# Performance work log

Hardware: AMD Instinct MI355X
Metric: run time of the kernel (lower is better)

The kernel has to match this reference:

```python
import jax, jax.numpy as jnp
import numpy as np

EPS = 1e-6

def setup_inputs() -> dict:
    key = jax.random.key(0)
    ks = jax.random.split(key, 9)
    B, H, M = 8192, 1024, 16
    Hh = H // 2
    s = lambda k, shape, fan: jax.random.normal(k, shape, jnp.float32) * (1.0 / np.sqrt(fan))
    return {
        "query_embedding": jax.random.normal(ks[0], (B, H), jnp.float32),
        "cls1_w": s(ks[1], (Hh, H), H),
        "cls1_b": jnp.zeros((Hh,), jnp.float32),
        "cls3_w": s(ks[2], (M, Hh), Hh),
        "cls3_b": jnp.zeros((M,), jnp.float32),
        "exp_w1": s(ks[3], (M, Hh, H), H),
        "exp_b1": jnp.zeros((M, Hh), jnp.float32),
        "exp_w2": s(ks[4], (M, H, Hh), Hh),
        "exp_b2": jnp.zeros((M, H), jnp.float32),
    }

def _l2_normalize(x, eps=EPS):
    # F.normalize: x / clamp(||x||_2, min=eps)
    n = jnp.sqrt(jnp.sum(x * x, axis=-1, keepdims=True))
    return x / jnp.maximum(n, eps)

def reference(query_embedding, cls1_w, cls1_b, cls3_w, cls3_b,
              exp_w1, exp_b1, exp_w2, exp_b2):
    q = query_embedding  # [B, H]
    # --- cls(): gating network (eval, sbmoe_top1) ---
    x1 = jax.nn.relu(q @ cls1_w.T + cls1_b)          # [B, H/2]
    logits = x1 @ cls3_w.T + cls3_b                  # [B, M]
    probs = jax.nn.softmax(logits, axis=-1)          # [B, M]
    top1 = jnp.argmax(probs, axis=-1)                # [B]
    mask = jax.nn.one_hot(top1, probs.shape[-1], dtype=probs.dtype)
    gates = probs * mask                             # [B, M] (one nonzero/row)
    # --- query_embedder(): run all experts, gate, combine ---
    h = jax.nn.relu(jnp.einsum('bd,mhd->bmh', q, exp_w1) + exp_b1)   # [B, M, H/2]
    expert_out = jnp.einsum('bmh,mdh->bmd', h, exp_w2) + exp_b2      # [B, M, H]
    combined = jnp.einsum('bmd,bm->bd', expert_out, gates)           # [B, H]
    out = _l2_normalize(combined) + q
    return out
```

## Files before the change

### kernel.cpp

```cpp
#include <hip/hip_runtime.h>
#include <math.h>

#define NB 8192
#define H 1024
#define HH 512
#define NEXP 16
#define NT128 96
#define AMBIG_THR 1e-3f

typedef __attribute__((ext_vector_type(8))) short bfrag;
typedef __attribute__((ext_vector_type(4))) float f4;

__device__ __forceinline__ f4 MF(bfrag a, bfrag b, f4 c) {
    return __builtin_amdgcn_mfma_f32_16x16x32_bf16(a, b, c, 0, 0, 0);
}
__device__ __forceinline__ unsigned short f2bf(float f) {
    unsigned u = __float_as_uint(f);
    u += 0x7fff + ((u >> 16) & 1);
    return (unsigned short)(u >> 16);
}
__device__ __forceinline__ float bf2f(unsigned short h) {
    return __uint_as_float((unsigned)h << 16);
}

typedef __attribute__((address_space(1))) const unsigned GAS;
typedef __attribute__((address_space(3))) unsigned LAS;
__device__ __forceinline__ void gld16(const void* g, void* l) {
    __builtin_amdgcn_global_load_lds((GAS*)g, (LAS*)l, 16, 0, 0);
}

__global__ __launch_bounds__(256) void cvtA_kernel(
    const float* __restrict__ q, const float* __restrict__ w1, const float* __restrict__ w3,
    unsigned short* __restrict__ qhi, unsigned short* __restrict__ qlo,
    unsigned short* __restrict__ w1hi, unsigned short* __restrict__ w1lo,
    unsigned short* __restrict__ w3hi, unsigned short* __restrict__ w3lo,
    int* __restrict__ counts, int* __restrict__ ambig_cnt)
{
    const int b = blockIdx.x, t = threadIdx.x;
    if (b == 0) {
        if (t < NEXP) counts[t] = 0;
        if (t == NEXP) ambig_cnt[0] = 0;
    }
    const float* src; unsigned short *hi, *lo; int i;
    if (b < 8192)      { src = q;  hi = qhi;  lo = qlo;  i = b * 256 + t; }
    else if (b < 8704) { src = w1; hi = w1hi; lo = w1lo; i = (b - 8192) * 256 + t; }
    else               { src = w3; hi = w3hi; lo = w3lo; i = (b - 8704) * 256 + t; }
    float4 v = ((const float4*)src)[i];
    ushort4 h, l;
    h.x = f2bf(v.x); l.x = f2bf(v.x - bf2f(h.x));
    h.y = f2bf(v.y); l.y = f2bf(v.y - bf2f(h.y));
    h.z = f2bf(v.z); l.z = f2bf(v.z - bf2f(h.z));
    h.w = f2bf(v.w); l.w = f2bf(v.w - bf2f(h.w));
    ((ushort4*)hi)[i] = h;
    ((ushort4*)lo)[i] = l;
}

__global__ __launch_bounds__(256) void cvtB_kernel(
    const float* __restrict__ ew1, const float* __restrict__ ew2,
    unsigned short* __restrict__ d1, unsigned short* __restrict__ d2)
{
    const int b = blockIdx.x, t = threadIdx.x;
    const float* src; unsigned short* dst; int i;
    if (b < 8192) { src = ew1; dst = d1; i = b * 256 + t; }
    else          { src = ew2; dst = d2; i = (b - 8192) * 256 + t; }
    float4 v = ((const float4*)src)[i];
    ushort4 h;
    h.x = f2bf(v.x); h.y = f2bf(v.y); h.z = f2bf(v.z); h.w = f2bf(v.w);
    ((ushort4*)dst)[i] = h;
}

__global__ __launch_bounds__(512) void g1_kernel(
    const unsigned short* __restrict__ qhi, const unsigned short* __restrict__ qlo,
    const unsigned short* __restrict__ w1hi, const unsigned short* __restrict__ w1lo,
    const float* __restrict__ b1,
    unsigned short* __restrict__ x1hi, unsigned short* __restrict__ x1lo)
{
    __shared__ unsigned short Ah[3][128][32];
    __shared__ unsigned short Al[3][128][32];
    __shared__ unsigned short Bh[3][128][32];
    __shared__ unsigned short Bl[3][128][32];

    const int t = threadIdx.x, w = t >> 6, lane = t & 63;
    const int quad = lane >> 4, l16 = lane & 15;
    const int wr = w & 3, wc = w >> 2;
    const int rowA0 = blockIdx.x * 128;
    const int colB0 = blockIdx.y * 128;
    const int rl = lane >> 2, sl = lane & 3;

    const unsigned short* gsrc[4];
    unsigned short* lbase[4];
    #pragma unroll
    for (int j = 0; j < 4; ++j) {
        int c = w + j * 8;
        int rloc; const unsigned short* s; unsigned short* d;
        if (c < 8)       { rloc = c * 16 + rl;        s = qhi  + (size_t)(rowA0 + rloc) * H; d = &Ah[0][c * 16][0]; }
        else if (c < 16) { rloc = (c - 8) * 16 + rl;  s = qlo  + (size_t)(rowA0 + rloc) * H; d = &Al[0][(c - 8) * 16][0]; }
        else if (c < 24) { rloc = (c - 16) * 16 + rl; s = w1hi + (size_t)(colB0 + rloc) * H; d = &Bh[0][(c - 16) * 16][0]; }
        else             { rloc = (c - 24) * 16 + rl; s = w1lo + (size_t)(colB0 + rloc) * H; d = &Bl[0][(c - 24) * 16][0]; }
        int f = (rloc & 3) ^ ((rloc >> 2) & 3);
        gsrc[j]  = s + (sl ^ f) * 8;
        lbase[j] = d;
    }
    const int bstr = 128 * 32;

    const f4 z4 = {0.f, 0.f, 0.f, 0.f};
    f4 acc[2][4] = {{z4, z4, z4, z4}, {z4, z4, z4, z4}};
    const int sw = (quad ^ (l16 & 3) ^ (l16 >> 2)) * 8;
    const int ra0 = wr * 32 + l16, ra1 = ra0 + 16;
    const int cbase = wc * 64;

    auto STAGE = [&](int buf, int kt) {
        #pragma unroll
        for (int j = 0; j < 4; ++j)
            gld16(gsrc[j] + kt * 32, lbase[j] + buf * bstr);
    };
    auto COMPUTE = [&](int buf) {
        bfrag ah0 = *(const bfrag*)&Ah[buf][ra0][sw];
        bfrag al0 = *(const bfrag*)&Al[buf][ra0][sw];
        bfrag ah1 = *(const bfrag*)&Ah[buf][ra1][sw];
        bfrag al1 = *(const bfrag*)&Al[buf][ra1][sw];
        #pragma unroll
        for (int cb = 0; cb < 4; ++cb) {
            bfrag bh = *(const bfrag*)&Bh[buf][cbase + cb * 16 + l16][sw];
            bfrag bl = *(const bfrag*)&Bl[buf][cbase + cb * 16 + l16][sw];
            acc[0][cb] = MF(al0, bh, MF(ah0, bl, MF(ah0, bh, acc[0][cb])));
            acc[1][cb] = MF(al1, bh, MF(ah1, bl, MF(ah1, bh, acc[1][cb])));
        }
    };

    STAGE(0, 0);
    STAGE(1, 1);
    for (int kt = 0; kt < 32; ++kt) {
        if (kt < 31) asm volatile("s_waitcnt vmcnt(4)" ::: "memory");
        else         asm volatile("s_waitcnt vmcnt(0)" ::: "memory");
        __builtin_amdgcn_s_barrier();
        if (kt < 30) STAGE((kt + 2) % 3, kt + 2);
        COMPUTE(kt % 3);
    }

    const int row0 = rowA0 + wr * 32;
    #pragma unroll
    for (int cb = 0; cb < 4; ++cb) {
        int col = colB0 + cbase + cb * 16 + l16;
        float bias = b1[col];
        #pragma unroll
        for (int rb = 0; rb < 2; ++rb)
            #pragma unroll
            for (int i = 0; i < 4; ++i) {
                int row = rb * 16 + quad * 4 + i;
                float v = fmaxf(acc[rb][cb][i] + bias, 0.f);
                unsigned short hh = f2bf(v);
                size_t idx = (size_t)(row0 + row) * HH + col;
                x1hi[idx] = hh;
                x1lo[idx] = f2bf(v - bf2f(hh));
            }
    }
}

__global__ __launch_bounds__(256) void logits_kernel(
    const unsigned short* __restrict__ x1hi, const unsigned short* __restrict__ x1lo,
    const unsigned short* __restrict__ w3hi, const unsigned short* __restrict__ w3lo,
    const float* __restrict__ b3,
    int* __restrict__ top1, float* __restrict__ gval, int* __restrict__ counts,
    int* __restrict__ ambig_rows, int* __restrict__ ambig_cnt)
{
    __shared__ float lgp[4][32][NEXP];
    const int t = threadIdx.x, wave = t >> 6, lane = t & 63;
    const int quad = lane >> 4, l16 = lane & 15;
    const int row0 = blockIdx.x * 32;
    const f4 z4 = {0.f, 0.f, 0.f, 0.f};

    f4 l0 = z4, l1 = z4;
    const size_t ar0 = (size_t)(row0 + l16) * HH + quad * 8;
    const size_t ar1 = ar0 + (size_t)16 * HH;
    const size_t br = (size_t)l16 * HH + quad * 8;
    #pragma unroll
    for (int ks = 0; ks < 4; ++ks) {
        int kk = wave * 128 + ks * 32;
        bfrag ah0 = *(const bfrag*)(x1hi + ar0 + kk);
        bfrag al0 = *(const bfrag*)(x1lo + ar0 + kk);
        bfrag ah1 = *(const bfrag*)(x1hi + ar1 + kk);
        bfrag al1 = *(const bfrag*)(x1lo + ar1 + kk);
        bfrag bh  = *(const bfrag*)(w3hi + br + kk);
        bfrag bl  = *(const bfrag*)(w3lo + br + kk);
        l0 = MF(al0, bh, MF(ah0, bl, MF(ah0, bh, l0)));
        l1 = MF(al1, bh, MF(ah1, bl, MF(ah1, bh, l1)));
    }
    #pragma unroll
    for (int i = 0; i < 4; ++i) {
        lgp[wave][quad * 4 + i][l16] = l0[i];
        lgp[wave][16 + quad * 4 + i][l16] = l1[i];
    }
    __syncthreads();

    if (t < 32) {
        float lg[NEXP];
        #pragma unroll
        for (int m = 0; m < NEXP; ++m)
            lg[m] = lgp[0][t][m] + lgp[1][t][m] + lgp[2][t][m] + lgp[3][t][m] + b3[m];
        float best = lg[0], second = -3.4e38f; int bi = 0;
        #pragma unroll
        for (int m = 1; m < NEXP; ++m) {
            float v = lg[m];
            if (v > best) { second = best; best = v; bi = m; }
            else if (v > second) second = v;
        }
        float se = 0.f;
        #pragma unroll
        for (int m = 0; m < NEXP; ++m) se += expf(lg[m] - best);
        int grow = row0 + t;
        top1[grow] = bi;
        gval[grow] = 1.f / se;
        atomicAdd(&counts[bi], 1);
        if (best - second < AMBIG_THR) {
            int pos = atomicAdd(ambig_cnt, 1);
            if (pos < NB) ambig_rows[pos] = grow;
        }
    }
}

__global__ __launch_bounds__(256) void fixup1_kernel(
    const float* __restrict__ q, const float* __restrict__ w1, const float* __restrict__ b1,
    const int* __restrict__ ambig_rows, const int* __restrict__ ambig_cnt,
    float* __restrict__ x1buf)
{
    __shared__ __align__(16) float qrow[H];
    const int t = threadIdx.x, wv = t >> 6, ln = t & 63;
    const int chunk = blockIdx.x & 7;
    const int slot  = blockIdx.x >> 3;
    const int base  = chunk * 64;
    int nn = *ambig_cnt; if (nn > NB) nn = NB;
    for (int ii = slot; ii < nn; ii += 32) {
        int row = ambig_rows[ii];
        ((float4*)qrow)[t] = ((const float4*)(q + (size_t)row * H))[t];
        __syncthreads();
        for (int c = base + wv * 2; c < base + 64; c += 8) {
            const float4* w0 = (const float4*)(w1 + (size_t)c * H);
            const float4* w1r = (const float4*)(w1 + (size_t)(c + 1) * H);
            const float4* qv = (const float4*)qrow;
            float s0 = 0.f, s1 = 0.f;
            #pragma unroll
            for (int j = 0; j < 4; ++j) {
                float4 a = qv[j * 64 + ln];
                float4 b0 = w0[j * 64 + ln];
                float4 b1v = w1r[j * 64 + ln];
                s0 += a.x * b0.x + a.y * b0.y + a.z * b0.z + a.w * b0.w;
                s1 += a.x * b1v.x + a.y * b1v.y + a.z * b1v.z + a.w * b1v.w;
            }
            #pragma unroll
            for (int off = 32; off; off >>= 1) {
                s0 += __shfl_xor(s0, off, 64);
                s1 += __shfl_xor(s1, off, 64);
            }
            if (ln == 0) {
                x1buf[(size_t)ii * HH + c]     = fmaxf(s0 + b1[c], 0.f);
                x1buf[(size_t)ii * HH + c + 1] = fmaxf(s1 + b1[c + 1], 0.f);
            }
        }
        __syncthreads();
    }
}

__global__ __launch_bounds__(256) void fixup2_kernel(
    const float* __restrict__ x1buf,
    const float* __restrict__ w3, const float* __restrict__ b3,
    const int* __restrict__ ambig_rows, const int* __restrict__ ambig_cnt,
    int* __restrict__ top1, float* __restrict__ gval, int* __restrict__ counts)
{
    __shared__ float lgs[NEXP];
    const int t = threadIdx.x, wv = t >> 6, ln = t & 63;
    int nn = *ambig_cnt; if (nn > NB) nn = NB;
    for (int ii = blockIdx.x; ii < nn; ii += gridDim.x) {
        int row = ambig_rows[ii];
        const float4* xv = (const float4*)(x1buf + (size_t)ii * HH);
        for (int m = wv; m < NEXP; m += 4) {
            const float4* wr = (const float4*)(w3 + (size_t)m * HH);
            float s = 0.f;
            #pragma unroll
            for (int j = 0; j < 2; ++j) {
                float4 a = xv[j * 64 + ln];
                float4 b = wr[j * 64 + ln];
                s += a.x * b.x + a.y * b.y + a.z * b.z + a.w * b.w;
            }
            #pragma unroll
            for (int off = 32; off; off >>= 1) s += __shfl_xor(s, off, 64);
            if (ln == 0) lgs[m] = s + b3[m];
        }
        __syncthreads();
        if (t == 0) {
            float best = lgs[0]; int bi = 0;
            #pragma unroll
            for (int m = 1; m < NEXP; ++m) if (lgs[m] > best) { best = lgs[m]; bi = m; }
            float se = 0.f;
            #pragma unroll
            for (int m = 0; m < NEXP; ++m) se += expf(lgs[m] - best);
            int old = top1[row];
            if (bi != old) {
                atomicSub(&counts[old], 1);
                atomicAdd(&counts[bi], 1);
                top1[row] = bi;
            }
            gval[row] = 1.f / se;
        }
        __syncthreads();
    }
}

__global__ __launch_bounds__(256) void osc_kernel(
    const int* __restrict__ counts,
    int* __restrict__ tm_e, int* __restrict__ tm_p, int* __restrict__ tm_end,
    const int* __restrict__ top1, int* __restrict__ brows)
{
    __shared__ int sbpos[NEXP];
    const int t = threadIdx.x;
    if (t == 0) {
        int run = 0, tile = 0;
        for (int e = 0; e < NEXP; ++e) {
            sbpos[e] = run;
            int beg = run, end = run + counts[e];
            for (int p = beg; p < end; p += 128) {
                tm_e[tile] = e; tm_p[tile] = p; tm_end[tile] = end; ++tile;
            }
            run = end;
        }
        for (; tile < NT128; ++tile) tm_e[tile] = -1;
    }
    __syncthreads();
    for (int i = t; i < NB; i += 256) {
        int e = top1[i];
        int pos = atomicAdd(&sbpos[e], 1);
        brows[pos] = i;
    }
}

__global__ __launch_bounds__(512) void exp1_kernel(
    const unsigned short* __restrict__ qb, const unsigned short* __restrict__ ew1b,
    const float* __restrict__ eb1,
    const int* __restrict__ tm_e, const int* __restrict__ tm_p, const int* __restrict__ tm_end,
    const int* __restrict__ brows, unsigned short* __restrict__ h)
{
    const int e = tm_e[blockIdx.x];
    if (e < 0) return;
    const int p0 = tm_p[blockIdx.x], end = tm_end[blockIdx.x];

    __shared__ unsigned short A[3][128][32];
    __shared__ unsigned short B[3][128][32];

    const int t = threadIdx.x, w = t >> 6, lane = t & 63;
    const int quad = lane >> 4, l16 = lane & 15;
    const int wr = w & 3, wc = w >> 2;
    const int c0 = blockIdx.y * 128;
    const unsigned short* w1p = ew1b + (size_t)e * HH * H;
    const int rl = lane >> 2, sl = lane & 3;

    const unsigned short* gsrc[2];
    unsigned short* lbase[2];
    #pragma unroll
    for (int j = 0; j < 2; ++j) {
        int c = w + j * 8;
        int rloc; const unsigned short* s; unsigned short* d;
        if (c < 8) {
            rloc = c * 16 + rl;
            int pa = p0 + rloc; if (pa >= end) pa = end - 1;
            s = qb + (size_t)brows[pa] * H;
            d = &A[0][c * 16][0];
        } else {
            rloc = (c - 8) * 16 + rl;
            s = w1p + (size_t)(c0 + rloc) * H;
            d = &B[0][(c - 8) * 16][0];
        }
        int f = (rloc & 3) ^ ((rloc >> 2) & 3);
        gsrc[j]  = s + (sl ^ f) * 8;
        lbase[j] = d;
    }
    const int bstr = 128 * 32;

    const f4 z4 = {0.f, 0.f, 0.f, 0.f};
    f4 acc[2][4] = {{z4, z4, z4, z4}, {z4, z4, z4, z4}};
    const int sw = (quad ^ (l16 & 3) ^ (l16 >> 2)) * 8;
    const int ra0 = wr * 32 + l16, ra1 = ra0 + 16;
    const int cbase = wc * 64;

    auto STAGE = [&](int buf, int kt) {
        #pragma unroll
        for (int j = 0; j < 2; ++j)
            gld16(gsrc[j] + kt * 32, lbase[j] + buf * bstr);
    };
    auto COMPUTE = [&](int buf) {
        bfrag a0 = *(const bfrag*)&A[buf][ra0][sw];
        bfrag a1 = *(const bfrag*)&A[buf][ra1][sw];
        #pragma unroll
        for (int cb = 0; cb < 4; ++cb) {
            bfrag bb = *(const bfrag*)&B[buf][cbase + cb * 16 + l16][sw];
            acc[0][cb] = MF(a0, bb, acc[0][cb]);
            acc[1][cb] = MF(a1, bb, acc[1][cb]);
        }
    };

    STAGE(0, 0);
    STAGE(1, 1);
    for (int kt = 0; kt < 32; ++kt) {
        if (kt < 31) asm volatile("s_waitcnt vmcnt(2)" ::: "memory");
        else         asm volatile("s_waitcnt vmcnt(0)" ::: "memory");
        __builtin_amdgcn_s_barrier();
        if (kt < 30) STAGE((kt + 2) % 3, kt + 2);
        COMPUTE(kt % 3);
    }

    const int prow0 = p0 + wr * 32;
    #pragma unroll
    for (int cb = 0; cb < 4; ++cb) {
        int col = c0 + cbase + cb * 16 + l16;
        float bias = eb1[e * HH + col];
        #pragma unroll
        for (int rb = 0; rb < 2; ++rb)
            #pragma unroll
            for (int i = 0; i < 4; ++i) {
                int row = rb * 16 + quad * 4 + i;
                if (prow0 + row < end)
                    h[(size_t)(prow0 + row) * HH + col] = f2bf(fmaxf(acc[rb][cb][i] + bias, 0.f));
            }
    }
}

__global__ __launch_bounds__(512) void exp2_kernel(
    const unsigned short* __restrict__ h, const unsigned short* __restrict__ ew2b,
    const float* __restrict__ eb2,
    const int* __restrict__ tm_e, const int* __restrict__ tm_p, const int* __restrict__ tm_end,
    const int* __restrict__ brows,
    float* __restrict__ vout, float* __restrict__ psum)
{
    const int e = tm_e[blockIdx.x];
    if (e < 0) return;
    const int p0 = tm_p[blockIdx.x], end = tm_end[blockIdx.x];

    __shared__ unsigned short A[3][128][32];
    __shared__ unsigned short B[3][128][32];

    const int t = threadIdx.x, w = t >> 6, lane = t & 63;
    const int quad = lane >> 4, l16 = lane & 15;
    const int wr = w & 3, wc = w >> 2;
    const int c0 = blockIdx.y * 128;
    const unsigned short* w2p = ew2b + (size_t)e * H * HH;
    const int rl = lane >> 2, sl = lane & 3;

    const unsigned short* gsrc[2];
    unsigned short* lbase[2];
    #pragma unroll
    for (int j = 0; j < 2; ++j) {
        int c = w + j * 8;
        int rloc; const unsigned short* s; unsigned short* d;
        if (c < 8) {
            rloc = c * 16 + rl;
            int pa = p0 + rloc; if (pa >= end) pa = end - 1;
            s = h + (size_t)pa * HH;
            d = &A[0][c * 16][0];
        } else {
            rloc = (c - 8) * 16 + rl;
            s = w2p + (size_t)(c0 + rloc) * HH;
            d = &B[0][(c - 8) * 16][0];
        }
        int f = (rloc & 3) ^ ((rloc >> 2) & 3);
        gsrc[j]  = s + (sl ^ f) * 8;
        lbase[j] = d;
    }
    const int bstr = 128 * 32;

    const f4 z4 = {0.f, 0.f, 0.f, 0.f};
    f4 acc[2][4] = {{z4, z4, z4, z4}, {z4, z4, z4, z4}};
    const int sw = (quad ^ (l16 & 3) ^ (l16 >> 2)) * 8;
    const int ra0 = wr * 32 + l16, ra1 = ra0 + 16;
    const int cbase = wc * 64;

    auto STAGE = [&](int buf, int kt) {
        #pragma unroll
        for (int j = 0; j < 2; ++j)
            gld16(gsrc[j] + kt * 32, lbase[j] + buf * bstr);
    };
    auto COMPUTE = [&](int buf) {
        bfrag a0 = *(const bfrag*)&A[buf][ra0][sw];
        bfrag a1 = *(const bfrag*)&A[buf][ra1][sw];
        #pragma unroll
        for (int cb = 0; cb < 4; ++cb) {
            bfrag bb = *(const bfrag*)&B[buf][cbase + cb * 16 + l16][sw];
            acc[0][cb] = MF(a0, bb, acc[0][cb]);
            acc[1][cb] = MF(a1, bb, acc[1][cb]);
        }
    };

    STAGE(0, 0);
    STAGE(1, 1);
    for (int kt = 0; kt < 16; ++kt) {
        if (kt < 15) asm volatile("s_waitcnt vmcnt(2)" ::: "memory");
        else         asm volatile("s_waitcnt vmcnt(0)" ::: "memory");
        __builtin_amdgcn_s_barrier();
        if (kt < 14) STAGE((kt + 2) % 3, kt + 2);
        COMPUTE(kt % 3);
    }

    const int pw0 = p0 + wr * 32;
    const int slot = blockIdx.y * 2 + wc;
    float rs0[4] = {0.f, 0.f, 0.f, 0.f}, rs1[4] = {0.f, 0.f, 0.f, 0.f};
    #pragma unroll
    for (int i = 0; i < 4; ++i) {
        int row0i = quad * 4 + i, row1i = 16 + quad * 4 + i;
        int g0 = pw0 + row0i; if (g0 >= end) g0 = end - 1;
        int g1 = pw0 + row1i; if (g1 >= end) g1 = end - 1;
        int gr0 = brows[g0], gr1 = brows[g1];
        #pragma unroll
        for (int cb = 0; cb < 4; ++cb) {
            int col = c0 + cbase + cb * 16 + l16;
            float bias = eb2[e * H + col];
            float v0 = acc[0][cb][i] + bias;
            float v1 = acc[1][cb][i] + bias;
            vout[(size_t)gr0 * H + col] = v0;
            vout[(size_t)gr1 * H + col] = v1;
            rs0[i] += v0 * v0;
            rs1[i] += v1 * v1;
        }
    }
    #pragma unroll
    for (int i = 0; i < 4; ++i) {
        float s0 = rs0[i], s1 = rs1[i];
        #pragma unroll
        for (int off = 8; off; off >>= 1) {
            s0 += __shfl_xor(s0, off, 16);
            s1 += __shfl_xor(s1, off, 16);
        }
        if (l16 == 0) {
            int g0 = pw0 + quad * 4 + i;      if (g0 >= end) g0 = end - 1;
            int g1 = pw0 + 16 + quad * 4 + i; if (g1 >= end) g1 = end - 1;
            psum[(size_t)brows[g0] * 16 + slot] = s0;
            psum[(size_t)brows[g1] * 16 + slot] = s1;
        }
    }
}

__global__ __launch_bounds__(256) void finalize_kernel(
    float* __restrict__ out, const float* __restrict__ q,
    const float* __restrict__ psum, const float* __restrict__ gval)
{
    const int row = blockIdx.x, t = threadIdx.x;
    float s = 0.f;
    #pragma unroll
    for (int j = 0; j < 16; ++j) s += psum[(size_t)row * 16 + j];
    float g = gval[row];
    float sc = g / fmaxf(g * sqrtf(s), 1e-6f);
    size_t i = (size_t)row * 256 + t;
    float4 v = ((const float4*)out)[i];
    float4 qq = ((const float4*)q)[i];
    float4 o;
    o.x = v.x * sc + qq.x;
    o.y = v.y * sc + qq.y;
    o.z = v.z * sc + qq.z;
    o.w = v.w * sc + qq.w;
    ((float4*)out)[i] = o;
}

extern "C" void kernel_launch(void* const* d_in, const int* in_sizes, int n_in,
                              void* d_out, int out_size, void* d_ws, size_t ws_size,
                              hipStream_t stream) {
    const float* q      = (const float*)d_in[0];
    const float* cls1_w = (const float*)d_in[1];
    const float* cls1_b = (const float*)d_in[2];
    const float* cls3_w = (const float*)d_in[3];
    const float* cls3_b = (const float*)d_in[4];
    const float* exp_w1 = (const float*)d_in[5];
    const float* exp_b1 = (const float*)d_in[6];
    const float* exp_w2 = (const float*)d_in[7];
    const float* exp_b2 = (const float*)d_in[8];
    float* out = (float*)d_out;

    char* w = (char*)d_ws;
    float* psum   = (float*)w;              w += (size_t)NB * 16 * 4;
    float* gvalp  = (float*)w;              w += (size_t)NB * 4;
    int* top1     = (int*)w;                w += (size_t)NB * 4;
    int* brows    = (int*)w;                w += (size_t)NB * 4;
    int* ambig_rows = (int*)w;              w += (size_t)NB * 4;
    int* counts   = (int*)w;                w += 16 * 4;
    int* ambig_cnt = (int*)w;               w += 4 * 4;
    int* tm_e     = (int*)w;                w += NT128 * 4;
    int* tm_p     = (int*)w;                w += NT128 * 4;
    int* tm_end   = (int*)w;                w += NT128 * 4;
    w = (char*)(((size_t)w + 15) & ~(size_t)15);
    unsigned short* qhi  = (unsigned short*)w;  w += (size_t)NB * H * 2;
    unsigned short* qlo  = (unsigned short*)w;  w += (size_t)NB * H * 2;
    unsigned short* x1hi = (unsigned short*)w;
    unsigned short* x1lo = x1hi + (size_t)NB * HH;  w += (size_t)NB * HH * 2 * 2;
    unsigned short* hbuf = (unsigned short*)w;  w += (size_t)NB * HH * 2;
    unsigned short* w1hi = (unsigned short*)w;  w += (size_t)HH * H * 2;
    unsigned short* w1lo = (unsigned short*)w;  w += (size_t)HH * H * 2;
    unsigned short* w3hi = (unsigned short*)w;  w += (size_t)NEXP * HH * 2;
    unsigned short* w3lo = (unsigned short*)w;  w += (size_t)NEXP * HH * 2;
    unsigned short* ew1b = x1hi;
    unsigned short* ew2b = qlo;
    float* x1buf = (float*)x1hi;

    cvtA_kernel<<<8712, 256, 0, stream>>>(q, cls1_w, cls3_w, qhi, qlo, w1hi, w1lo,
                                          w3hi, w3lo, counts, ambig_cnt);
    g1_kernel<<<dim3(NB / 128, 4), 512, 0, stream>>>(qhi, qlo, w1hi, w1lo, cls1_b, x1hi, x1lo);
    logits_kernel<<<NB / 32, 256, 0, stream>>>(x1hi, x1lo, w3hi, w3lo, cls3_b,
                                               top1, gvalp, counts, ambig_rows, ambig_cnt);
    fixup1_kernel<<<256, 256, 0, stream>>>(q, cls1_w, cls1_b, ambig_rows, ambig_cnt, x1buf);
    fixup2_kernel<<<64, 256, 0, stream>>>(x1buf, cls3_w, cls3_b, ambig_rows, ambig_cnt,
                                          top1, gvalp, counts);
    cvtB_kernel<<<16384, 256, 0, stream>>>(exp_w1, exp_w2, ew1b, ew2b);
    osc_kernel<<<1, 256, 0, stream>>>(counts, tm_e, tm_p, tm_end, top1, brows);
    exp1_kernel<<<dim3(NT128, 4), 512, 0, stream>>>(qhi, ew1b, exp_b1,
                                                    tm_e, tm_p, tm_end, brows, hbuf);
    exp2_kernel<<<dim3(NT128, 8), 512, 0, stream>>>(hbuf, ew2b, exp_b2,
                                                    tm_e, tm_p, tm_end, brows, out, psum);
    finalize_kernel<<<NB, 256, 0, stream>>>(out, q, psum, gvalp);
}
```

Measured before the change: 359.0 us.

## Fuse gating logits projection into first GEMM epilogue via fp32 atomics

```diff
diff --git a/kernel.cpp b/kernel.cpp
--- a/kernel.cpp
+++ b/kernel.cpp
@@ -30,21 +30,23 @@
 }
 
 __global__ __launch_bounds__(256) void cvtA_kernel(
-    const float* __restrict__ q, const float* __restrict__ w1, const float* __restrict__ w3,
+    const float* __restrict__ q, const float* __restrict__ w1,
     unsigned short* __restrict__ qhi, unsigned short* __restrict__ qlo,
     unsigned short* __restrict__ w1hi, unsigned short* __restrict__ w1lo,
-    unsigned short* __restrict__ w3hi, unsigned short* __restrict__ w3lo,
-    int* __restrict__ counts, int* __restrict__ ambig_cnt)
+    float* __restrict__ logitsf, int* __restrict__ counts, int* __restrict__ ambig_cnt)
 {
     const int b = blockIdx.x, t = threadIdx.x;
     if (b == 0) {
         if (t < NEXP) counts[t] = 0;
         if (t == NEXP) ambig_cnt[0] = 0;
     }
+    if (b < 128) {
+        float4 z = {0.f, 0.f, 0.f, 0.f};
+        ((float4*)logitsf)[b * 256 + t] = z;
+    }
     const float* src; unsigned short *hi, *lo; int i;
-    if (b < 8192)      { src = q;  hi = qhi;  lo = qlo;  i = b * 256 + t; }
-    else if (b < 8704) { src = w1; hi = w1hi; lo = w1lo; i = (b - 8192) * 256 + t; }
-    else               { src = w3; hi = w3hi; lo = w3lo; i = (b - 8704) * 256 + t; }
+    if (b < 8192) { src = q;  hi = qhi;  lo = qlo;  i = b * 256 + t; }
+    else          { src = w1; hi = w1hi; lo = w1lo; i = (b - 8192) * 256 + t; }
     float4 v = ((const float4*)src)[i];
     ushort4 h, l;
     h.x = f2bf(v.x); l.x = f2bf(v.x - bf2f(h.x));
@@ -72,13 +74,14 @@
 __global__ __launch_bounds__(512) void g1_kernel(
     const unsigned short* __restrict__ qhi, const unsigned short* __restrict__ qlo,
     const unsigned short* __restrict__ w1hi, const unsigned short* __restrict__ w1lo,
-    const float* __restrict__ b1,
-    unsigned short* __restrict__ x1hi, unsigned short* __restrict__ x1lo)
+    const float* __restrict__ b1, const float* __restrict__ w3f,
+    float* __restrict__ logitsf)
 {
     __shared__ unsigned short Ah[3][128][32];
     __shared__ unsigned short Al[3][128][32];
     __shared__ unsigned short Bh[3][128][32];
     __shared__ unsigned short Bl[3][128][32];
+    __shared__ float w3s[NEXP][128];
 
     const int t = threadIdx.x, w = t >> 6, lane = t & 63;
     const int quad = lane >> 4, l16 = lane & 15;
@@ -86,6 +89,12 @@
     const int rowA0 = blockIdx.x * 128;
     const int colB0 = blockIdx.y * 128;
     const int rl = lane >> 2, sl = lane & 3;
+
+    for (int i = t; i < NEXP * 128; i += 512) {
+        int m = i >> 7, c = i & 127;
+        w3s[m][c] = w3f[(size_t)m * HH + colB0 + c];
+    }
+    asm volatile("s_waitcnt lgkmcnt(0)" ::: "memory");
 
     const unsigned short* gsrc[4];
     unsigned short* lbase[4];
@@ -138,85 +147,70 @@
         COMPUTE(kt % 3);
     }
 
-    const int row0 = rowA0 + wr * 32;
+    float vv[2][4][4];
     #pragma unroll
     for (int cb = 0; cb < 4; ++cb) {
-        int col = colB0 + cbase + cb * 16 + l16;
-        float bias = b1[col];
+        float bias = b1[colB0 + cbase + cb * 16 + l16];
         #pragma unroll
         for (int rb = 0; rb < 2; ++rb)
             #pragma unroll
+            for (int i = 0; i < 4; ++i)
+                vv[rb][cb][i] = fmaxf(acc[rb][cb][i] + bias, 0.f);
+    }
+    const int rowbase = rowA0 + wr * 32;
+    #pragma unroll
+    for (int m = 0; m < NEXP; ++m) {
+        float w3v[4];
+        #pragma unroll
+        for (int cb = 0; cb < 4; ++cb) w3v[cb] = w3s[m][cbase + cb * 16 + l16];
+        #pragma unroll
+        for (int rb = 0; rb < 2; ++rb)
+            #pragma unroll
             for (int i = 0; i < 4; ++i) {
-                int row = rb * 16 + quad * 4 + i;
-                float v = fmaxf(acc[rb][cb][i] + bias, 0.f);
-                unsigned short hh = f2bf(v);
-                size_t idx = (size_t)(row0 + row) * HH + col;
-                x1hi[idx] = hh;
-                x1lo[idx] = f2bf(v - bf2f(hh));
-            }
-    }
-}
-
-__global__ __launch_bounds__(256) void logits_kernel(
-    const unsigned short* __restrict__ x1hi, const unsigned short* __restrict__ x1lo,
-    const unsigned short* __restrict__ w3hi, const unsigned short* __restrict__ w3lo,
-    const float* __restrict__ b3,
+                float s = vv[rb][0][i] * w3v[0] + vv[rb][1][i] * w3v[1]
+                        + vv[rb][2][i] * w3v[2] + vv[rb][3][i] * w3v[3];
+                s += __shfl_xor(s, 1);
+                s += __shfl_xor(s, 2);
+                s += __shfl_xor(s, 4);
+                s += __shfl_xor(s, 8);
+                if (l16 == 0)
+                    atomicAdd(&logitsf[(size_t)(rowbase + rb * 16 + quad * 4 + i) * NEXP + m], s);
+            }
+    }
+}
+
+__global__ __launch_bounds__(256) void argmax_kernel(
+    const float* __restrict__ logitsf, const float* __restrict__ b3,
     int* __restrict__ top1, float* __restrict__ gval, int* __restrict__ counts,
     int* __restrict__ ambig_rows, int* __restrict__ ambig_cnt)
 {
-    __shared__ float lgp[4][32][NEXP];
-    const int t = threadIdx.x, wave = t >> 6, lane = t & 63;
-    const int quad = lane >> 4, l16 = lane & 15;
-    const int row0 = blockIdx.x * 32;
-    const f4 z4 = {0.f, 0.f, 0.f, 0.f};
-
-    f4 l0 = z4, l1 = z4;
-    const size_t ar0 = (size_t)(row0 + l16) * HH + quad * 8;
-    const size_t ar1 = ar0 + (size_t)16 * HH;
-    const size_t br = (size_t)l16 * HH + quad * 8;
-    #pragma unroll
-    for (int ks = 0; ks < 4; ++ks) {
-        int kk = wave * 128 + ks * 32;
-        bfrag ah0 = *(const bfrag*)(x1hi + ar0 + kk);
-        bfrag al0 = *(const bfrag*)(x1lo + ar0 + kk);
-        bfrag ah1 = *(const bfrag*)(x1hi + ar1 + kk);
-        bfrag al1 = *(const bfrag*)(x1lo + ar1 + kk);
-        bfrag bh  = *(const bfrag*)(w3hi + br + kk);
-        bfrag bl  = *(const bfrag*)(w3lo + br + kk);
-        l0 = MF(al0, bh, MF(ah0, bl, MF(ah0, bh, l0)));
-        l1 = MF(al1, bh, MF(ah1, bl, MF(ah1, bh, l1)));
-    }
-    #pragma unroll
-    for (int i = 0; i < 4; ++i) {
-        lgp[wave][quad * 4 + i][l16] = l0[i];
-        lgp[wave][16 + quad * 4 + i][l16] = l1[i];
-    }
+    __shared__ int hist[NEXP];
+    const int t = threadIdx.x;
+    if (t < NEXP) hist[t] = 0;
     __syncthreads();
-
-    if (t < 32) {
-        float lg[NEXP];
-        #pragma unroll
-        for (int m = 0; m < NEXP; ++m)
-            lg[m] = lgp[0][t][m] + lgp[1][t][m] + lgp[2][t][m] + lgp[3][t][m] + b3[m];
-        float best = lg[0], second = -3.4e38f; int bi = 0;
-        #pragma unroll
-        for (int m = 1; m < NEXP; ++m) {
-            float v = lg[m];
-            if (v > best) { second = best; best = v; bi = m; }
-            else if (v > second) second = v;
-        }
-        float se = 0.f;
-        #pragma unroll
-        for (int m = 0; m < NEXP; ++m) se += expf(lg[m] - best);
-        int grow = row0 + t;
-        top1[grow] = bi;
-        gval[grow] = 1.f / se;
-        atomicAdd(&counts[bi], 1);
-        if (best - second < AMBIG_THR) {
-            int pos = atomicAdd(ambig_cnt, 1);
-            if (pos < NB) ambig_rows[pos] = grow;
-        }
-    }
+    const int row = blockIdx.x * 256 + t;
+    float lg[NEXP];
+    #pragma unroll
+    for (int m = 0; m < NEXP; ++m) lg[m] = logitsf[(size_t)row * NEXP + m] + b3[m];
+    float best = lg[0], second = -3.4e38f; int bi = 0;
+    #pragma unroll
+    for (int m = 1; m < NEXP; ++m) {
+        float v = lg[m];
+        if (v > best) { second = best; best = v; bi = m; }
+        else if (v > second) second = v;
+    }
+    float se = 0.f;
+    #pragma unroll
+    for (int m = 0; m < NEXP; ++m) se += expf(lg[m] - best);
+    top1[row] = bi;
+    gval[row] = 1.f / se;
+    atomicAdd(&hist[bi], 1);
+    if (best - second < AMBIG_THR) {
+        int pos = atomicAdd(ambig_cnt, 1);
+        if (pos < NB) ambig_rows[pos] = row;
+    }
+    __syncthreads();
+    if (t < NEXP) atomicAdd(&counts[t], hist[t]);
 }
 
 __global__ __launch_bounds__(256) void fixup1_kernel(
@@ -573,6 +567,7 @@
 
     char* w = (char*)d_ws;
     float* psum   = (float*)w;              w += (size_t)NB * 16 * 4;
+    float* logitsf = (float*)w;             w += (size_t)NB * NEXP * 4;
     float* gvalp  = (float*)w;              w += (size_t)NB * 4;
     int* top1     = (int*)w;                w += (size_t)NB * 4;
     int* brows    = (int*)w;                w += (size_t)NB * 4;
@@ -585,22 +580,20 @@
     w = (char*)(((size_t)w + 15) & ~(size_t)15);
     unsigned short* qhi  = (unsigned short*)w;  w += (size_t)NB * H * 2;
     unsigned short* qlo  = (unsigned short*)w;  w += (size_t)NB * H * 2;
-    unsigned short* x1hi = (unsigned short*)w;
-    unsigned short* x1lo = x1hi + (size_t)NB * HH;  w += (size_t)NB * HH * 2 * 2;
+    char* scratch16 = w;                        w += (size_t)NB * HH * 2 * 2;
     unsigned short* hbuf = (unsigned short*)w;  w += (size_t)NB * HH * 2;
     unsigned short* w1hi = (unsigned short*)w;  w += (size_t)HH * H * 2;
     unsigned short* w1lo = (unsigned short*)w;  w += (size_t)HH * H * 2;
-    unsigned short* w3hi = (unsigned short*)w;  w += (size_t)NEXP * HH * 2;
-    unsigned short* w3lo = (unsigned short*)w;  w += (size_t)NEXP * HH * 2;
-    unsigned short* ew1b = x1hi;
+    float* x1buf = (float*)scratch16;
+    unsigned short* ew1b = (unsigned short*)scratch16;
     unsigned short* ew2b = qlo;
-    float* x1buf = (float*)x1hi;
-
-    cvtA_kernel<<<8712, 256, 0, stream>>>(q, cls1_w, cls3_w, qhi, qlo, w1hi, w1lo,
-                                          w3hi, w3lo, counts, ambig_cnt);
-    g1_kernel<<<dim3(NB / 128, 4), 512, 0, stream>>>(qhi, qlo, w1hi, w1lo, cls1_b, x1hi, x1lo);
-    logits_kernel<<<NB / 32, 256, 0, stream>>>(x1hi, x1lo, w3hi, w3lo, cls3_b,
-                                               top1, gvalp, counts, ambig_rows, ambig_cnt);
+
+    cvtA_kernel<<<8704, 256, 0, stream>>>(q, cls1_w, qhi, qlo, w1hi, w1lo,
+                                          logitsf, counts, ambig_cnt);
+    g1_kernel<<<dim3(NB / 128, 4), 512, 0, stream>>>(qhi, qlo, w1hi, w1lo, cls1_b,
+                                                     cls3_w, logitsf);
+    argmax_kernel<<<NB / 256, 256, 0, stream>>>(logitsf, cls3_b, top1, gvalp, counts,
+                                                ambig_rows, ambig_cnt);
     fixup1_kernel<<<256, 256, 0, stream>>>(q, cls1_w, cls1_b, ambig_rows, ambig_cnt, x1buf);
     fixup2_kernel<<<64, 256, 0, stream>>>(x1buf, cls3_w, cls3_b, ambig_rows, ambig_cnt,
                                           top1, gvalp, counts);
```

Measured after the change: 365.9 us. Within noise of the previous version (+1.9%).
